# Kernel optimization log

Measured on AMD Instinct MI355X. Metric: run time of the kernel, lower is better.

## Reference

```python
import jax, jax.numpy as jnp
import numpy as np

T, E, IN, OUT, A, R = 16384, 8, 1024, 1024, 8, 16  # tokens, experts, d_in, d_out, adapters, lora rank


def prepare_routing(x, indices, num_groups):
    """Sort tokens by group index; return sorted x, per-group counts, unsort map, sorted ids."""
    sort_idx = jnp.argsort(indices)  # stable sort keeps within-group order
    x_sorted = x[sort_idx]
    group_sizes = jnp.bincount(indices, length=num_groups).astype(jnp.int32)
    unsort_indices = jnp.argsort(sort_idx)
    return x_sorted, group_sizes, unsort_indices, indices[sort_idx]


def setup_inputs() -> dict:
    key = jax.random.key(0)
    ks = jax.random.split(key, 6)
    # tokens pre-sorted by expert: group_sizes must sum to T exactly
    expert_ids = jnp.sort(jax.random.randint(ks[0], (T,), 0, E))
    group_sizes = jnp.bincount(expert_ids, length=E).astype(jnp.int32)
    x = jax.random.normal(ks[1], (T, IN), jnp.float32)
    adapter_indices_sorted = jax.random.randint(ks[2], (T,), 0, A)
    weight = jax.random.normal(ks[3], (E, IN, OUT), jnp.float32) * 0.02
    lora_A = jax.random.normal(ks[4], (A, E, IN, R), jnp.float32) * 0.02
    lora_B = jax.random.normal(ks[5], (A, E, R, OUT), jnp.float32) * 0.02
    lora_scaling = jnp.ones((A,), jnp.float32)
    return {
        "x": x,
        "group_sizes": group_sizes,
        "adapter_indices_sorted": adapter_indices_sorted,
        "weight": weight,
        "lora_A": lora_A,
        "lora_B": lora_B,
        "lora_scaling": lora_scaling,
    }


def reference(x, group_sizes, adapter_indices_sorted, weight, lora_A, lora_B, lora_scaling):
    # base grouped GEMM over experts: [T,IN] x [E,IN,OUT] -> [T,OUT]
    base_out = jax.lax.ragged_dot(x, weight, group_sizes)

    # per-token expert id from contiguous group sizes
    expert_ids = jnp.repeat(jnp.arange(E), group_sizes, total_repeat_length=T)
    flattened = expert_ids * A + adapter_indices_sorted  # expert-major (E,A) group id

    # flatten adapters x experts into E*A groups (expert-major to match flattened ids)
    A_mat = lora_A.transpose(1, 0, 2, 3).reshape(E * A, IN, R)
    B_mat = lora_B.transpose(1, 0, 2, 3).reshape(E * A, R, OUT)

    x_sorted, combined_gs, unsort_indices, _ = prepare_routing(x, flattened, E * A)
    inter = jax.lax.ragged_dot(x_sorted, A_mat, combined_gs)          # [T,R]
    lora_out_sorted = jax.lax.ragged_dot(inter, B_mat, combined_gs)   # [T,OUT]
    lora_out = lora_out_sorted[unsort_indices]
    lora_out = lora_out * lora_scaling[adapter_indices_sorted][:, None]
    return base_out + lora_out
```

## Files before the change

### kernel.cpp

```cpp
#include <hip/hip_runtime.h>

#define T_TOK 16384
#define NEXP 8
#define DIN 1024
#define DOUT 1024
#define NADP 8
#define RANK 16
#define NGRP 64
#define MAXTILES 135
#define TILE2 64
#define MAXT2 320

typedef float f32x4 __attribute__((ext_vector_type(4)));
typedef __bf16 bf16x8 __attribute__((ext_vector_type(8)));

typedef __attribute__((address_space(3))) void lds_void;
typedef __attribute__((address_space(1))) void g_void;

static __device__ __forceinline__ unsigned short f2bf(float f) {
    union { float f; unsigned u; } c; c.f = f;
    unsigned r = c.u + 0x7FFFu + ((c.u >> 16) & 1u);
    return (unsigned short)(r >> 16);
}

#define NBX 16512
#define NBW 2048
__global__ __launch_bounds__(256) void k_convert_all(const float* __restrict__ x,
                                                     const float* __restrict__ W,
                                                     const float* __restrict__ lA,
                                                     unsigned short* __restrict__ xb,
                                                     unsigned short* __restrict__ Wt,
                                                     unsigned short* __restrict__ Agt) {
    __shared__ __attribute__((aligned(16))) unsigned short lds_u[16 * 1032];
    int b = blockIdx.x;
    int t = threadIdx.x;
    if (b < NBX) {
        size_t i = ((size_t)b * 256 + t) * 4;
        ushort4 u;
        if (i < (size_t)T_TOK * DIN) {
            float4 v = *(const float4*)(x + i);
            u.x = f2bf(v.x); u.y = f2bf(v.y); u.z = f2bf(v.z); u.w = f2bf(v.w);
        } else {
            u.x = 0; u.y = 0; u.z = 0; u.w = 0;
        }
        *(ushort4*)(xb + i) = u;
    } else if (b < NBX + NBW) {
        int idx = b - NBX;
        int e = idx >> 8;
        int k0 = ((idx >> 4) & 15) * 64, n0 = (idx & 15) * 64;
        const float* We = W + (size_t)e * DIN * DOUT;
        unsigned short* Wte = Wt + (size_t)e * DIN * DOUT;
        int kr = t >> 2;
        int nc = (t & 3) * 16;
#pragma unroll
        for (int j = 0; j < 4; j++) {
            float4 v = *(const float4*)(We + (size_t)(k0 + kr) * DOUT + n0 + nc + j * 4);
            lds_u[(nc + j * 4 + 0) * 80 + kr] = f2bf(v.x);
            lds_u[(nc + j * 4 + 1) * 80 + kr] = f2bf(v.y);
            lds_u[(nc + j * 4 + 2) * 80 + kr] = f2bf(v.z);
            lds_u[(nc + j * 4 + 3) * 80 + kr] = f2bf(v.w);
        }
        __syncthreads();
        int n = t >> 2;
        int kk = (t & 3) * 16;
        uint4 v0 = *(const uint4*)&lds_u[n * 80 + kk];
        uint4 v1 = *(const uint4*)&lds_u[n * 80 + kk + 8];
        *(uint4*)(Wte + (size_t)(n0 + n) * DIN + k0 + kk) = v0;
        *(uint4*)(Wte + (size_t)(n0 + n) * DIN + k0 + kk + 8) = v1;
    } else {
        int g = b - (NBX + NBW);
        int a = g & 7, e = g >> 3;
        const float* src = lA + (size_t)(a * NEXP + e) * DIN * RANK;
#pragma unroll
        for (int it = 0; it < 4; it++) {
            int k = it * 256 + t;
            const float4* p = (const float4*)(src + (size_t)k * RANK);
            float4 v0 = p[0], v1 = p[1], v2 = p[2], v3 = p[3];
            lds_u[0 * 1032 + k] = f2bf(v0.x);  lds_u[1 * 1032 + k] = f2bf(v0.y);
            lds_u[2 * 1032 + k] = f2bf(v0.z);  lds_u[3 * 1032 + k] = f2bf(v0.w);
            lds_u[4 * 1032 + k] = f2bf(v1.x);  lds_u[5 * 1032 + k] = f2bf(v1.y);
            lds_u[6 * 1032 + k] = f2bf(v1.z);  lds_u[7 * 1032 + k] = f2bf(v1.w);
            lds_u[8 * 1032 + k] = f2bf(v2.x);  lds_u[9 * 1032 + k] = f2bf(v2.y);
            lds_u[10 * 1032 + k] = f2bf(v2.z); lds_u[11 * 1032 + k] = f2bf(v2.w);
            lds_u[12 * 1032 + k] = f2bf(v3.x); lds_u[13 * 1032 + k] = f2bf(v3.y);
            lds_u[14 * 1032 + k] = f2bf(v3.z); lds_u[15 * 1032 + k] = f2bf(v3.w);
        }
        __syncthreads();
        unsigned short* dst = Agt + (size_t)g * RANK * DIN;
        int r = t >> 4, ks = (t & 15) * 64;
#pragma unroll
        for (int j = 0; j < 8; j++)
            *(uint4*)(dst + r * DIN + ks + j * 8) = *(const uint4*)&lds_u[r * 1032 + ks + j * 8];
    }
}

__global__ __launch_bounds__(1024) void k_route_all(const int* __restrict__ gs,
                                                    const int* __restrict__ aidx,
                                                    int* __restrict__ gid,
                                                    int* __restrict__ perm,
                                                    int* __restrict__ sched,
                                                    int* __restrict__ sched2) {
    __shared__ int hist[NGRP];
    __shared__ int cursor[NGRP];
    __shared__ int ebase[NEXP + 1];
    int t = threadIdx.x;
    if (t < NGRP) hist[t] = 0;
    if (t == 0) {
        int acc = 0;
        for (int i = 0; i < NEXP; i++) { ebase[i] = acc; acc += gs[i]; }
        ebase[NEXP] = acc;
    }
    __syncthreads();
    for (int i = 0; i < T_TOK / 1024; i++) {
        int tok = i * 1024 + t;
        int e = 0;
#pragma unroll
        for (int j = 1; j < NEXP; j++) e += (tok >= ebase[j]);
        int g = e * NADP + aidx[tok];
        gid[tok] = g;
        atomicAdd(&hist[g], 1);
    }
    if (t < 128) perm[T_TOK + t] = T_TOK;
    __syncthreads();
    if (t == 0) {
        int off = 0, tc = 0;
        for (int g = 0; g < NGRP; g++) {
            cursor[g] = off;
            int sz = hist[g];
            for (int m = 0; m < sz; m += TILE2) {
                sched2[tc * 4 + 0] = g;
                sched2[tc * 4 + 1] = off + m;
                sched2[tc * 4 + 2] = (sz - m) < TILE2 ? (sz - m) : TILE2;
                sched2[tc * 4 + 3] = 0;
                tc++;
            }
            off += sz;
        }
        for (; tc < MAXT2; tc++) {
            sched2[tc * 4 + 0] = 0; sched2[tc * 4 + 1] = 0;
            sched2[tc * 4 + 2] = 0; sched2[tc * 4 + 3] = 0;
        }
    } else if (t == 64) {
        int off = 0, tc = 0;
        for (int e = 0; e < NEXP; e++) {
            int sz = ebase[e + 1] - ebase[e];
            for (int m = 0; m < sz; m += 128) {
                sched[tc * 4 + 0] = e;
                sched[tc * 4 + 1] = off + m;
                sched[tc * 4 + 2] = (sz - m) < 128 ? (sz - m) : 128;
                sched[tc * 4 + 3] = 0;
                tc++;
            }
            off += sz;
        }
        for (; tc < MAXTILES; tc++) {
            sched[tc * 4 + 0] = 0; sched[tc * 4 + 1] = 0;
            sched[tc * 4 + 2] = 0; sched[tc * 4 + 3] = 0;
        }
    }
    __syncthreads();
    for (int i = 0; i < T_TOK / 1024; i++) {
        int tok = i * 1024 + t;
        int pos = atomicAdd(&cursor[gid[tok]], 1);
        perm[pos] = tok;
    }
}

__global__ __launch_bounds__(256) void k_gemm(const unsigned short* __restrict__ xb,
                                              const unsigned short* __restrict__ wt,
                                              const int* __restrict__ sched,
                                              float* __restrict__ out) {
    __shared__ __attribute__((aligned(16))) unsigned short As[128 * 32];
    __shared__ __attribute__((aligned(16))) unsigned short Bs[128 * 32];
    int e     = sched[blockIdx.y * 4 + 0];
    int m0    = sched[blockIdx.y * 4 + 1];
    int valid = sched[blockIdx.y * 4 + 2];
    if (valid == 0) return;
    int n0 = blockIdx.x * 128;

    int t = threadIdx.x;
    int lane = t & 63;
    int wave = t >> 6;
    int wm = wave >> 1, wn = wave & 1;
    int ln = lane & 15, q = lane >> 4;

    const unsigned short* wte = wt + (size_t)e * DIN * DOUT;

    f32x4 acc[4][4];
#pragma unroll
    for (int i = 0; i < 4; i++)
#pragma unroll
        for (int j = 0; j < 4; j++) acc[i][j] = (f32x4){0.f, 0.f, 0.f, 0.f};

    int c0 = t, c1 = t + 256;

    for (int k0 = 0; k0 < DIN; k0 += 32) {
        __syncthreads();
        {
            const unsigned short* ga0 = xb + (size_t)(m0 + (c0 >> 2)) * DIN + k0 + (c0 & 3) * 8;
            const unsigned short* ga1 = xb + (size_t)(m0 + (c1 >> 2)) * DIN + k0 + (c1 & 3) * 8;
            __builtin_amdgcn_global_load_lds((const g_void*)ga0, (lds_void*)((char*)As + wave * 1024), 16, 0, 0);
            __builtin_amdgcn_global_load_lds((const g_void*)ga1, (lds_void*)((char*)As + 4096 + wave * 1024), 16, 0, 0);
            const unsigned short* gb0 = wte + (size_t)(n0 + (c0 >> 2)) * DIN + k0 + (c0 & 3) * 8;
            const unsigned short* gb1 = wte + (size_t)(n0 + (c1 >> 2)) * DIN + k0 + (c1 & 3) * 8;
            __builtin_amdgcn_global_load_lds((const g_void*)gb0, (lds_void*)((char*)Bs + wave * 1024), 16, 0, 0);
            __builtin_amdgcn_global_load_lds((const g_void*)gb1, (lds_void*)((char*)Bs + 4096 + wave * 1024), 16, 0, 0);
        }
        __syncthreads();
        bf16x8 af[4], bfr[4];
#pragma unroll
        for (int mi = 0; mi < 4; mi++)
            af[mi] = *(const bf16x8*)((const char*)As + ((wm * 64 + mi * 16 + ln) * 64 + q * 16));
#pragma unroll
        for (int ni = 0; ni < 4; ni++)
            bfr[ni] = *(const bf16x8*)((const char*)Bs + ((wn * 64 + ni * 16 + ln) * 64 + q * 16));
#pragma unroll
        for (int mi = 0; mi < 4; mi++)
#pragma unroll
            for (int ni = 0; ni < 4; ni++)
                acc[mi][ni] = __builtin_amdgcn_mfma_f32_16x16x32_bf16(af[mi], bfr[ni], acc[mi][ni], 0, 0, 0);
    }

#pragma unroll
    for (int mi = 0; mi < 4; mi++) {
#pragma unroll
        for (int r = 0; r < 4; r++) {
            int row_l = wm * 64 + mi * 16 + q * 4 + r;
            if (row_l < valid) {
                float* orow = out + (size_t)(m0 + row_l) * DOUT + n0 + wn * 64 + ln;
#pragma unroll
                for (int ni = 0; ni < 4; ni++)
                    orow[ni * 16] = acc[mi][ni][r];
            }
        }
    }
}

__global__ __launch_bounds__(256) void k_pass1(const unsigned short* __restrict__ xb,
                                               const unsigned short* __restrict__ Agt,
                                               const int* __restrict__ sched2,
                                               const int* __restrict__ perm,
                                               float* __restrict__ inter) {
    __shared__ __attribute__((aligned(16))) unsigned short As[64 * 32];
    int g     = sched2[blockIdx.x * 4 + 0];
    int m0    = sched2[blockIdx.x * 4 + 1];
    int valid = sched2[blockIdx.x * 4 + 2];
    if (valid == 0) return;

    int t = threadIdx.x;
    int lane = t & 63, w = t >> 6;
    int ln = lane & 15, q = lane >> 4;

    const unsigned short* Ag = Agt + (size_t)g * RANK * DIN;
    int prow = perm[m0 + (t >> 2)];
    const unsigned short* ga_base = xb + (size_t)prow * DIN + (t & 3) * 8;

    f32x4 acc = (f32x4){0.f, 0.f, 0.f, 0.f};

    for (int k0 = 0; k0 < DIN; k0 += 32) {
        __syncthreads();
        __builtin_amdgcn_global_load_lds((const g_void*)(ga_base + k0),
                                         (lds_void*)((char*)As + w * 1024), 16, 0, 0);
        __syncthreads();
        bf16x8 bfr = *(const bf16x8*)(Ag + ln * DIN + k0 + q * 8);
        bf16x8 af  = *(const bf16x8*)((const char*)As + ((w * 16 + ln) * 64 + q * 16));
        acc = __builtin_amdgcn_mfma_f32_16x16x32_bf16(af, bfr, acc, 0, 0, 0);
    }
#pragma unroll
    for (int r = 0; r < 4; r++) {
        int row = w * 16 + q * 4 + r;
        if (row < valid)
            inter[(size_t)(m0 + row) * RANK + ln] = acc[r];
    }
}

__global__ __launch_bounds__(256) void k_pass2(const float* __restrict__ inter,
                                               const int* __restrict__ sched2,
                                               const int* __restrict__ perm,
                                               const int* __restrict__ aidx,
                                               const float* __restrict__ lB,
                                               const float* __restrict__ scal,
                                               float* __restrict__ out) {
    __shared__ float Bsm[RANK * 256];
    __shared__ float ism[TILE2 * RANK];
    __shared__ float ssm[TILE2];
    __shared__ int   ptm[TILE2];
    int g     = sched2[blockIdx.x * 4 + 0];
    int m0    = sched2[blockIdx.x * 4 + 1];
    int valid = sched2[blockIdx.x * 4 + 2];
    if (valid == 0) return;
    int n0 = blockIdx.y * 256;
    int a = g & 7, e = g >> 3;
    int t = threadIdx.x;

    {
        const float* Bsrc = lB + ((size_t)(a * NEXP + e) * RANK + (t >> 4)) * DOUT + n0 + (t & 15) * 16;
        float* Bdst = &Bsm[(t >> 4) * 256 + (t & 15) * 16];
#pragma unroll
        for (int j = 0; j < 4; j++)
            *(float4*)(Bdst + j * 4) = *(const float4*)(Bsrc + j * 4);
    }
    {
        int tok = t >> 2, part = t & 3;
        int p = (tok < valid) ? perm[m0 + tok] : 0;
        if (part == 0) {
            ptm[tok] = p;
            ssm[tok] = (tok < valid) ? scal[aidx[p]] : 0.f;
        }
        int srow = (tok < valid) ? (m0 + tok) : m0;
        *(float4*)&ism[tok * RANK + part * 4] = *(const float4*)(inter + (size_t)srow * RANK + part * 4);
    }
    __syncthreads();

    int lane = t & 63, w = t >> 6;
#pragma unroll 1
    for (int tk = 0; tk < 16; tk++) {
        int tok = w * 16 + tk;
        if (tok >= valid) continue;
        float s = ssm[tok];
        const float* ir = &ism[tok * RANK];
        float* orow = out + (size_t)ptm[tok] * DOUT + n0 + lane;
#pragma unroll
        for (int c = 0; c < 4; c++) {
            const float* bcol = &Bsm[lane + c * 64];
            float v = 0.f;
#pragma unroll
            for (int r = 0; r < RANK; r++)
                v += ir[r] * bcol[r * 256];
            orow[c * 64] += s * v;
        }
    }
}

extern "C" void kernel_launch(void* const* d_in, const int* in_sizes, int n_in,
                              void* d_out, int out_size, void* d_ws, size_t ws_size,
                              hipStream_t stream) {
    (void)in_sizes; (void)n_in; (void)out_size; (void)ws_size;
    const float* x    = (const float*)d_in[0];
    const int*   gs   = (const int*)d_in[1];
    const int*   aidx = (const int*)d_in[2];
    const float* W    = (const float*)d_in[3];
    const float* lA   = (const float*)d_in[4];
    const float* lB   = (const float*)d_in[5];
    const float* scal = (const float*)d_in[6];
    float* out = (float*)d_out;

    char* ws = (char*)d_ws;
    unsigned short* xb    = (unsigned short*)ws;            size_t o = 33816576;
    unsigned short* wt    = (unsigned short*)(ws + o);      o += 16777216;
    unsigned short* Agt   = (unsigned short*)(ws + o);      o += 2097152;
    float*          inter = (float*)(ws + o);               o += 1048576;
    int*            sched = (int*)(ws + o);                 o += 2176;
    int*            sched2= (int*)(ws + o);                 o += 5120;
    int*            gid   = (int*)(ws + o);                 o += 65536;
    int*            perm  = (int*)(ws + o);                 o += 66048;

    k_convert_all<<<NBX + NBW + NGRP, 256, 0, stream>>>(x, W, lA, xb, wt, Agt);
    k_route_all<<<1, 1024, 0, stream>>>(gs, aidx, gid, perm, sched, sched2);
    k_gemm<<<dim3(8, MAXTILES), 256, 0, stream>>>(xb, wt, sched, out);
    k_pass1<<<MAXT2, 256, 0, stream>>>(xb, Agt, sched2, perm, inter);
    k_pass2<<<dim3(MAXT2, 4), 256, 0, stream>>>(inter, sched2, perm, aidx, lB, scal, out);
}
```

Baseline: 318.8 us.

## Fuse LoRA-B projection into base grouped GEMM epilogue via block-sparse MFMA

Removes the separate LoRA pass2 kernel. pass1 now scatters the rank-16 intermediates back into token order, and the base GEMM appends a K=128 MFMA stage. In that stage the scaled intermediate is placed into an adapter-indexed slot of a zero-filled LDS tile and multiplied by a pre-transposed bf16 lora_B laid out per expert as [OUT, A*R]. This avoids a second read-modify-write of the output and the scalar fp32 FMA loop. The base GEMM also moves to BK=64 with XOR-swizzled LDS, and a new conversion branch transposes lora_B to bf16. The trade-offs are extra MFMA work on mostly zero data, lora_B precision reduced to bf16, and the GEMM now depending on pass1.

```diff
diff --git a/kernel.cpp b/kernel.cpp
--- a/kernel.cpp
+++ b/kernel.cpp
@@ -10,6 +10,7 @@
 #define MAXTILES 135
 #define TILE2 64
 #define MAXT2 320
+#define BK 64
 
 typedef float f32x4 __attribute__((ext_vector_type(4)));
 typedef __bf16 bf16x8 __attribute__((ext_vector_type(8)));
@@ -28,9 +29,11 @@
 __global__ __launch_bounds__(256) void k_convert_all(const float* __restrict__ x,
                                                      const float* __restrict__ W,
                                                      const float* __restrict__ lA,
+                                                     const float* __restrict__ lB,
                                                      unsigned short* __restrict__ xb,
                                                      unsigned short* __restrict__ Wt,
-                                                     unsigned short* __restrict__ Agt) {
+                                                     unsigned short* __restrict__ Agt,
+                                                     unsigned short* __restrict__ Blt) {
     __shared__ __attribute__((aligned(16))) unsigned short lds_u[16 * 1032];
     int b = blockIdx.x;
     int t = threadIdx.x;
@@ -67,7 +70,7 @@
         uint4 v1 = *(const uint4*)&lds_u[n * 80 + kk + 8];
         *(uint4*)(Wte + (size_t)(n0 + n) * DIN + k0 + kk) = v0;
         *(uint4*)(Wte + (size_t)(n0 + n) * DIN + k0 + kk + 8) = v1;
-    } else {
+    } else if (b < NBX + NBW + NGRP) {
         int g = b - (NBX + NBW);
         int a = g & 7, e = g >> 3;
         const float* src = lA + (size_t)(a * NEXP + e) * DIN * RANK;
@@ -91,6 +94,41 @@
 #pragma unroll
         for (int j = 0; j < 8; j++)
             *(uint4*)(dst + r * DIN + ks + j * 8) = *(const uint4*)&lds_u[r * 1032 + ks + j * 8];
+    } else {
+        int idx = b - (NBX + NBW + NGRP);
+        int e = idx >> 3, nc = idx & 7;
+        int k = t >> 1, half = t & 1;
+        int a = k >> 4, r = k & 15;
+        const float* src = lB + ((size_t)(a * NEXP + e) * RANK + r) * DOUT + nc * 128 + half * 64;
+#pragma unroll
+        for (int j = 0; j < 16; j++) {
+            float4 v = *(const float4*)(src + j * 4);
+            int nl = half * 64 + j * 4;
+            lds_u[k * 129 + nl + 0] = f2bf(v.x);
+            lds_u[k * 129 + nl + 1] = f2bf(v.y);
+            lds_u[k * 129 + nl + 2] = f2bf(v.z);
+            lds_u[k * 129 + nl + 3] = f2bf(v.w);
+        }
+        __syncthreads();
+        int nl = t >> 1, kh = t & 1;
+        unsigned short* dst = Blt + ((size_t)(e * 1024 + nc * 128 + nl)) * 128 + kh * 64;
+#pragma unroll
+        for (int g2 = 0; g2 < 8; g2++) {
+            uint4 pv;
+            unsigned short s0 = lds_u[(kh * 64 + g2 * 8 + 0) * 129 + nl];
+            unsigned short s1 = lds_u[(kh * 64 + g2 * 8 + 1) * 129 + nl];
+            unsigned short s2 = lds_u[(kh * 64 + g2 * 8 + 2) * 129 + nl];
+            unsigned short s3 = lds_u[(kh * 64 + g2 * 8 + 3) * 129 + nl];
+            unsigned short s4 = lds_u[(kh * 64 + g2 * 8 + 4) * 129 + nl];
+            unsigned short s5 = lds_u[(kh * 64 + g2 * 8 + 5) * 129 + nl];
+            unsigned short s6 = lds_u[(kh * 64 + g2 * 8 + 6) * 129 + nl];
+            unsigned short s7 = lds_u[(kh * 64 + g2 * 8 + 7) * 129 + nl];
+            pv.x = (unsigned)s0 | ((unsigned)s1 << 16);
+            pv.y = (unsigned)s2 | ((unsigned)s3 << 16);
+            pv.z = (unsigned)s4 | ((unsigned)s5 << 16);
+            pv.w = (unsigned)s6 | ((unsigned)s7 << 16);
+            *(uint4*)(dst + g2 * 8) = pv;
+        }
     }
 }
 
@@ -166,76 +204,6 @@
     }
 }
 
-__global__ __launch_bounds__(256) void k_gemm(const unsigned short* __restrict__ xb,
-                                              const unsigned short* __restrict__ wt,
-                                              const int* __restrict__ sched,
-                                              float* __restrict__ out) {
-    __shared__ __attribute__((aligned(16))) unsigned short As[128 * 32];
-    __shared__ __attribute__((aligned(16))) unsigned short Bs[128 * 32];
-    int e     = sched[blockIdx.y * 4 + 0];
-    int m0    = sched[blockIdx.y * 4 + 1];
-    int valid = sched[blockIdx.y * 4 + 2];
-    if (valid == 0) return;
-    int n0 = blockIdx.x * 128;
-
-    int t = threadIdx.x;
-    int lane = t & 63;
-    int wave = t >> 6;
-    int wm = wave >> 1, wn = wave & 1;
-    int ln = lane & 15, q = lane >> 4;
-
-    const unsigned short* wte = wt + (size_t)e * DIN * DOUT;
-
-    f32x4 acc[4][4];
-#pragma unroll
-    for (int i = 0; i < 4; i++)
-#pragma unroll
-        for (int j = 0; j < 4; j++) acc[i][j] = (f32x4){0.f, 0.f, 0.f, 0.f};
-
-    int c0 = t, c1 = t + 256;
-
-    for (int k0 = 0; k0 < DIN; k0 += 32) {
-        __syncthreads();
-        {
-            const unsigned short* ga0 = xb + (size_t)(m0 + (c0 >> 2)) * DIN + k0 + (c0 & 3) * 8;
-            const unsigned short* ga1 = xb + (size_t)(m0 + (c1 >> 2)) * DIN + k0 + (c1 & 3) * 8;
-            __builtin_amdgcn_global_load_lds((const g_void*)ga0, (lds_void*)((char*)As + wave * 1024), 16, 0, 0);
-            __builtin_amdgcn_global_load_lds((const g_void*)ga1, (lds_void*)((char*)As + 4096 + wave * 1024), 16, 0, 0);
-            const unsigned short* gb0 = wte + (size_t)(n0 + (c0 >> 2)) * DIN + k0 + (c0 & 3) * 8;
-            const unsigned short* gb1 = wte + (size_t)(n0 + (c1 >> 2)) * DIN + k0 + (c1 & 3) * 8;
-            __builtin_amdgcn_global_load_lds((const g_void*)gb0, (lds_void*)((char*)Bs + wave * 1024), 16, 0, 0);
-            __builtin_amdgcn_global_load_lds((const g_void*)gb1, (lds_void*)((char*)Bs + 4096 + wave * 1024), 16, 0, 0);
-        }
-        __syncthreads();
-        bf16x8 af[4], bfr[4];
-#pragma unroll
-        for (int mi = 0; mi < 4; mi++)
-            af[mi] = *(const bf16x8*)((const char*)As + ((wm * 64 + mi * 16 + ln) * 64 + q * 16));
-#pragma unroll
-        for (int ni = 0; ni < 4; ni++)
-            bfr[ni] = *(const bf16x8*)((const char*)Bs + ((wn * 64 + ni * 16 + ln) * 64 + q * 16));
-#pragma unroll
-        for (int mi = 0; mi < 4; mi++)
-#pragma unroll
-            for (int ni = 0; ni < 4; ni++)
-                acc[mi][ni] = __builtin_amdgcn_mfma_f32_16x16x32_bf16(af[mi], bfr[ni], acc[mi][ni], 0, 0, 0);
-    }
-
-#pragma unroll
-    for (int mi = 0; mi < 4; mi++) {
-#pragma unroll
-        for (int r = 0; r < 4; r++) {
-            int row_l = wm * 64 + mi * 16 + q * 4 + r;
-            if (row_l < valid) {
-                float* orow = out + (size_t)(m0 + row_l) * DOUT + n0 + wn * 64 + ln;
-#pragma unroll
-                for (int ni = 0; ni < 4; ni++)
-                    orow[ni * 16] = acc[mi][ni][r];
-            }
-        }
-    }
-}
-
 __global__ __launch_bounds__(256) void k_pass1(const unsigned short* __restrict__ xb,
                                                const unsigned short* __restrict__ Agt,
                                                const int* __restrict__ sched2,
@@ -269,65 +237,142 @@
 #pragma unroll
     for (int r = 0; r < 4; r++) {
         int row = w * 16 + q * 4 + r;
-        if (row < valid)
-            inter[(size_t)(m0 + row) * RANK + ln] = acc[r];
-    }
-}
-
-__global__ __launch_bounds__(256) void k_pass2(const float* __restrict__ inter,
-                                               const int* __restrict__ sched2,
-                                               const int* __restrict__ perm,
-                                               const int* __restrict__ aidx,
-                                               const float* __restrict__ lB,
-                                               const float* __restrict__ scal,
-                                               float* __restrict__ out) {
-    __shared__ float Bsm[RANK * 256];
-    __shared__ float ism[TILE2 * RANK];
-    __shared__ float ssm[TILE2];
-    __shared__ int   ptm[TILE2];
-    int g     = sched2[blockIdx.x * 4 + 0];
-    int m0    = sched2[blockIdx.x * 4 + 1];
-    int valid = sched2[blockIdx.x * 4 + 2];
+        if (row < valid) {
+            int ptok = perm[m0 + row];
+            inter[(size_t)ptok * RANK + ln] = acc[r];
+        }
+    }
+}
+
+__global__ __launch_bounds__(256) void k_gemm(const unsigned short* __restrict__ xb,
+                                              const unsigned short* __restrict__ wt,
+                                              const int* __restrict__ sched,
+                                              const float* __restrict__ inter,
+                                              const int* __restrict__ aidx,
+                                              const float* __restrict__ scal,
+                                              const unsigned short* __restrict__ Blt,
+                                              float* __restrict__ out) {
+    __shared__ __attribute__((aligned(16))) unsigned short smem[128 * 128];
+    unsigned short* As = smem;
+    unsigned short* Bs = smem + 8192;
+    int e     = sched[blockIdx.y * 4 + 0];
+    int m0    = sched[blockIdx.y * 4 + 1];
+    int valid = sched[blockIdx.y * 4 + 2];
     if (valid == 0) return;
-    int n0 = blockIdx.y * 256;
-    int a = g & 7, e = g >> 3;
+    int n0 = blockIdx.x * 128;
+
     int t = threadIdx.x;
-
+    int lane = t & 63;
+    int wave = t >> 6;
+    int wm = wave >> 1, wn = wave & 1;
+    int ln = lane & 15, q = lane >> 4;
+
+    const unsigned short* wte = wt + (size_t)e * DIN * DOUT;
+
+    f32x4 acc[4][4];
+#pragma unroll
+    for (int i = 0; i < 4; i++)
+#pragma unroll
+        for (int j = 0; j < 4; j++) acc[i][j] = (f32x4){0.f, 0.f, 0.f, 0.f};
+
+    int srow[4], skoff[4];
+#pragma unroll
+    for (int j = 0; j < 4; j++) {
+        srow[j]  = j * 32 + wave * 8 + (lane >> 3);
+        skoff[j] = ((lane & 7) ^ (srow[j] & 7)) * 8;
+    }
+
+    for (int k0 = 0; k0 < DIN; k0 += BK) {
+        __syncthreads();
+#pragma unroll
+        for (int j = 0; j < 4; j++) {
+            __builtin_amdgcn_global_load_lds(
+                (const g_void*)(xb + (size_t)(m0 + srow[j]) * DIN + k0 + skoff[j]),
+                (lds_void*)((char*)As + j * 4096 + wave * 1024), 16, 0, 0);
+            __builtin_amdgcn_global_load_lds(
+                (const g_void*)(wte + (size_t)(n0 + srow[j]) * DIN + k0 + skoff[j]),
+                (lds_void*)((char*)Bs + j * 4096 + wave * 1024), 16, 0, 0);
+        }
+        __syncthreads();
+#pragma unroll
+        for (int kf = 0; kf < 2; kf++) {
+            bf16x8 af[4], bfr[4];
+#pragma unroll
+            for (int mi = 0; mi < 4; mi++) {
+                int row = wm * 64 + mi * 16 + ln;
+                int slot = (kf * 4 + q) ^ (ln & 7);
+                af[mi] = *(const bf16x8*)((const char*)As + row * 128 + slot * 16);
+            }
+#pragma unroll
+            for (int ni = 0; ni < 4; ni++) {
+                int row = wn * 64 + ni * 16 + ln;
+                int slot = (kf * 4 + q) ^ (ln & 7);
+                bfr[ni] = *(const bf16x8*)((const char*)Bs + row * 128 + slot * 16);
+            }
+#pragma unroll
+            for (int mi = 0; mi < 4; mi++)
+#pragma unroll
+                for (int ni = 0; ni < 4; ni++)
+                    acc[mi][ni] = __builtin_amdgcn_mfma_f32_16x16x32_bf16(af[mi], bfr[ni], acc[mi][ni], 0, 0, 0);
+        }
+    }
+
+    __syncthreads();
     {
-        const float* Bsrc = lB + ((size_t)(a * NEXP + e) * RANK + (t >> 4)) * DOUT + n0 + (t & 15) * 16;
-        float* Bdst = &Bsm[(t >> 4) * 256 + (t & 15) * 16];
-#pragma unroll
-        for (int j = 0; j < 4; j++)
-            *(float4*)(Bdst + j * 4) = *(const float4*)(Bsrc + j * 4);
-    }
+        uint4 z = {0u, 0u, 0u, 0u};
+#pragma unroll
+        for (int j = 0; j < 8; j++)
+            *(uint4*)((char*)smem + (j * 256 + t) * 16) = z;
+    }
+    __syncthreads();
     {
-        int tok = t >> 2, part = t & 3;
-        int p = (tok < valid) ? perm[m0 + tok] : 0;
-        if (part == 0) {
-            ptm[tok] = p;
-            ssm[tok] = (tok < valid) ? scal[aidx[p]] : 0.f;
-        }
-        int srow = (tok < valid) ? (m0 + tok) : m0;
-        *(float4*)&ism[tok * RANK + part * 4] = *(const float4*)(inter + (size_t)srow * RANK + part * 4);
-    }
-    __syncthreads();
-
-    int lane = t & 63, w = t >> 6;
-#pragma unroll 1
-    for (int tk = 0; tk < 16; tk++) {
-        int tok = w * 16 + tk;
-        if (tok >= valid) continue;
-        float s = ssm[tok];
-        const float* ir = &ism[tok * RANK];
-        float* orow = out + (size_t)ptm[tok] * DOUT + n0 + lane;
-#pragma unroll
-        for (int c = 0; c < 4; c++) {
-            const float* bcol = &Bsm[lane + c * 64];
-            float v = 0.f;
-#pragma unroll
-            for (int r = 0; r < RANK; r++)
-                v += ir[r] * bcol[r * 256];
-            orow[c * 64] += s * v;
+        int row = t >> 1, h = t & 1;
+        if (row < valid) {
+            int tok = m0 + row;
+            int a = aidx[tok];
+            float s = scal[a];
+            const float* ip = inter + (size_t)tok * RANK + h * 8;
+            float4 v0 = *(const float4*)ip;
+            float4 v1 = *(const float4*)(ip + 4);
+            unsigned short u[8];
+            u[0] = f2bf(s * v0.x); u[1] = f2bf(s * v0.y); u[2] = f2bf(s * v0.z); u[3] = f2bf(s * v0.w);
+            u[4] = f2bf(s * v1.x); u[5] = f2bf(s * v1.y); u[6] = f2bf(s * v1.z); u[7] = f2bf(s * v1.w);
+            int slot = (a * 2 + h) ^ (row & 15);
+            *(uint4*)((char*)smem + row * 256 + slot * 16) = *(uint4*)u;
+        }
+    }
+    __syncthreads();
+#pragma unroll
+    for (int kf = 0; kf < 4; kf++) {
+        bf16x8 af[4], bfr[4];
+        const unsigned short* bbase = Blt + ((size_t)(e * 1024 + n0 + wn * 64 + ln)) * 128 + kf * 32 + q * 8;
+#pragma unroll
+        for (int ni = 0; ni < 4; ni++)
+            bfr[ni] = *(const bf16x8*)(bbase + (size_t)ni * 16 * 128);
+#pragma unroll
+        for (int mi = 0; mi < 4; mi++) {
+            int row = wm * 64 + mi * 16 + ln;
+            int slot = (kf * 4 + q) ^ ln;
+            af[mi] = *(const bf16x8*)((const char*)smem + row * 256 + slot * 16);
+        }
+#pragma unroll
+        for (int mi = 0; mi < 4; mi++)
+#pragma unroll
+            for (int ni = 0; ni < 4; ni++)
+                acc[mi][ni] = __builtin_amdgcn_mfma_f32_16x16x32_bf16(af[mi], bfr[ni], acc[mi][ni], 0, 0, 0);
+    }
+
+#pragma unroll
+    for (int mi = 0; mi < 4; mi++) {
+#pragma unroll
+        for (int r = 0; r < 4; r++) {
+            int row_l = wm * 64 + mi * 16 + q * 4 + r;
+            if (row_l < valid) {
+                float* orow = out + (size_t)(m0 + row_l) * DOUT + n0 + wn * 64 + ln;
+#pragma unroll
+                for (int ni = 0; ni < 4; ni++)
+                    orow[ni * 16] = acc[mi][ni][r];
+            }
         }
     }
 }
@@ -349,15 +394,15 @@
     unsigned short* xb    = (unsigned short*)ws;            size_t o = 33816576;
     unsigned short* wt    = (unsigned short*)(ws + o);      o += 16777216;
     unsigned short* Agt   = (unsigned short*)(ws + o);      o += 2097152;
+    unsigned short* Blt   = (unsigned short*)(ws + o);      o += 2097152;
     float*          inter = (float*)(ws + o);               o += 1048576;
     int*            sched = (int*)(ws + o);                 o += 2176;
     int*            sched2= (int*)(ws + o);                 o += 5120;
     int*            gid   = (int*)(ws + o);                 o += 65536;
     int*            perm  = (int*)(ws + o);                 o += 66048;
 
-    k_convert_all<<<NBX + NBW + NGRP, 256, 0, stream>>>(x, W, lA, xb, wt, Agt);
+    k_convert_all<<<NBX + NBW + NGRP + 64, 256, 0, stream>>>(x, W, lA, lB, xb, wt, Agt, Blt);
     k_route_all<<<1, 1024, 0, stream>>>(gs, aidx, gid, perm, sched, sched2);
-    k_gemm<<<dim3(8, MAXTILES), 256, 0, stream>>>(xb, wt, sched, out);
     k_pass1<<<MAXT2, 256, 0, stream>>>(xb, Agt, sched2, perm, inter);
-    k_pass2<<<dim3(MAXT2, 4), 256, 0, stream>>>(inter, sched2, perm, aidx, lB, scal, out);
-}
+    k_gemm<<<dim3(8, MAXTILES), 256, 0, stream>>>(xb, wt, sched, inter, aidx, scal, Blt, out);
+}
```

New measurement: 294.7 us. 7.6% less time.
